# Optimization experiments

Measured on AMD Instinct MI355X. Metric: run time of the kernel, lower is better.

The kernel has to match this reference:

```python
import jax, jax.numpy as jnp
import numpy as np

M = 8192          # flattened tokens (batch*seq)
IN_FEATURES = 4096
OUT_FEATURES = 4096


def setup_inputs() -> dict:
    key = jax.random.key(0)
    k1, k2, k3 = jax.random.split(key, 3)
    # int8-valued activations and weights, stored as int32 (values in [-128, 127])
    x = jax.random.randint(k1, (M, IN_FEATURES), -128, 128, dtype=jnp.int32)
    int_weight = jax.random.randint(k2, (OUT_FEATURES, IN_FEATURES), -128, 127, dtype=jnp.int32)
    bias = (jax.random.normal(k3, (OUT_FEATURES,), dtype=jnp.float32) * 0.02).astype(jnp.float16)
    return {"x": x, "int_weight": int_weight, "bias": bias}


def reference(x, int_weight, bias):
    # x.to(torch.int8); quik int8Matmul: int8 GEMM with int32 accumulation, out = x @ W^T
    x_i8 = x.astype(jnp.int8)
    w_i8 = int_weight.astype(jnp.int8)
    acc = jax.lax.dot_general(
        x_i8, w_i8,
        dimension_numbers=(((1,), (1,)), ((), ())),  # [M, K] x [N, K] -> [M, N]
        preferred_element_type=jnp.int32,
    )
    # .to(torch.float16) then bias add (fused epilogue target)
    return acc.astype(jnp.float16) + bias
```

## Files before the change

### kernel.cpp

```cpp
#include <hip/hip_runtime.h>

#define MDIM 8192
#define NDIM 4096
#define KDIM 4096
#define BM 256
#define BN 128
#define BK 128

typedef int v4i __attribute__((ext_vector_type(4)));
typedef int v16i __attribute__((ext_vector_type(16)));

__device__ __forceinline__ unsigned pack4(int x, int y, int z, int w) {
    return (unsigned)(x & 0xff) | ((unsigned)(y & 0xff) << 8) |
           ((unsigned)(z & 0xff) << 16) | ((unsigned)w << 24);
}

__global__ __launch_bounds__(256) void pack_tiled(const int* __restrict__ x,
                                                  const int* __restrict__ w,
                                                  uint4* __restrict__ xp,
                                                  uint4* __restrict__ wp) {
    __shared__ unsigned lds32[256 * 33];
    const int wg  = blockIdx.x;
    const int tid = threadIdx.x;
    const int kq   = tid & 31;
    const int rsub = tid >> 5;

    if (wg < 1024) {
        const int mtile = wg >> 5, kiter = wg & 31;
        const int* base = x + (size_t)(mtile * 256) * KDIM + kiter * 128;
#pragma unroll
        for (int it = 0; it < 32; ++it) {
            const int row = it * 8 + rsub;
            int4 v = *(const int4*)(base + (size_t)row * KDIM + kq * 4);
            lds32[row * 33 + kq] = pack4(v.x, v.y, v.z, v.w);
        }
        __syncthreads();
        uint4* dst = xp + (size_t)(mtile * 32 + kiter) * 2048;
#pragma unroll
        for (int it = 0; it < 8; ++it) {
            const int g = it * 256 + tid;
            const int kb = g >> 8, row = g & 255;
            const unsigned* p = &lds32[row * 33 + kb * 4];
            uint4 o;
            o.x = p[0]; o.y = p[1]; o.z = p[2]; o.w = p[3];
            dst[g] = o;
        }
    } else {
        const int ntile = (wg - 1024) >> 5, kiter = wg & 31;
        const int* base = w + (size_t)(ntile * 128) * KDIM + kiter * 128;
#pragma unroll
        for (int it = 0; it < 16; ++it) {
            const int row = it * 8 + rsub;
            int4 v = *(const int4*)(base + (size_t)row * KDIM + kq * 4);
            lds32[row * 33 + kq] = pack4(v.x, v.y, v.z, v.w);
        }
        __syncthreads();
        uint4* dst = wp + (size_t)(ntile * 32 + kiter) * 1024;
#pragma unroll
        for (int it = 0; it < 4; ++it) {
            const int g  = it * 256 + tid;
            const int ln = g & 63, h = g >> 6;
            const int wc2 = h >> 3, nt = (h >> 2) & 1, ks = h & 3;
            const int row = wc2 * 64 + nt * 32 + (ln & 31);
            const int kb  = 2 * ks + (ln >> 5);
            const unsigned* p = &lds32[row * 33 + kb * 4];
            uint4 o;
            o.x = p[0]; o.y = p[1]; o.z = p[2]; o.w = p[3];
            dst[g] = o;
        }
    }
}

template <bool PACKED>
__global__ __launch_bounds__(256, 2) void gemm_i8(const char* __restrict__ Ap,
                                                  const char* __restrict__ Bp,
                                                  const int* __restrict__ A32,
                                                  const int* __restrict__ B32,
                                                  const _Float16* __restrict__ bias,
                                                  _Float16* __restrict__ out) {
    __shared__ char lds[65536];

    const int tid  = threadIdx.x;
    const int lane = tid & 63;
    const int wave = tid >> 6;
    const int bm0 = blockIdx.y * BM;
    const int bn0 = blockIdx.x * BN;
    const int wr  = wave >> 1;
    const int wc  = wave & 1;
    const int l31 = lane & 31;
    const int kg  = lane >> 5;

    const char* apan = Ap + (size_t)blockIdx.y * (BM * KDIM) + lane * 16;
    const char* bpan = Bp + (size_t)blockIdx.x * (BN * KDIM) + wc * 8192 + lane * 16;

    int abase[4];
#pragma unroll
    for (int mt = 0; mt < 4; ++mt)
        abase[mt] = kg * 4096 + (wr * 128 + mt * 32 + l31) * 16;

    v16i acc[4][2];
#pragma unroll
    for (int mt = 0; mt < 4; ++mt)
#pragma unroll
        for (int nt = 0; nt < 2; ++nt)
#pragma unroll
            for (int i = 0; i < 16; ++i) acc[mt][nt][i] = 0;

    auto issueA = [&](char* buf, const char* pan) {
#pragma unroll
        for (int r = 0; r < 8; ++r) {
            const int c = r * 4 + wave;
            __builtin_amdgcn_global_load_lds(
                (__attribute__((address_space(1))) void*)(pan + c * 1024),
                (__attribute__((address_space(3))) void*)(buf + c * 1024), 16, 0, 0);
        }
    };
    auto loadB = [&](v4i (&bf)[2][4], const char* pan) {
#pragma unroll
        for (int nt = 0; nt < 2; ++nt)
#pragma unroll
            for (int ks = 0; ks < 4; ++ks)
                bf[nt][ks] = *(const v4i*)(pan + (nt * 4 + ks) * 1024);
    };
    auto compute = [&](const char* buf, const v4i (&bf)[2][4]) {
#pragma unroll
        for (int ks = 0; ks < 4; ++ks) {
            v4i af[4];
#pragma unroll
            for (int mt = 0; mt < 4; ++mt)
                af[mt] = *(const v4i*)(buf + abase[mt] + ks * 8192);
#pragma unroll
            for (int mt = 0; mt < 4; ++mt)
#pragma unroll
                for (int nt = 0; nt < 2; ++nt)
                    acc[mt][nt] = __builtin_amdgcn_mfma_i32_32x32x32_i8(
                        af[mt], bf[nt][ks], acc[mt][nt], 0, 0, 0);
        }
    };

    if constexpr (PACKED) {
        v4i bf0[2][4], bf1[2][4];
        issueA(lds, apan);
        apan += BM * BK;
        loadB(bf0, bpan);
        bpan += BN * BK;
#pragma unroll 1
        for (int p = 0; p < 15; ++p) {
            __syncthreads();
            issueA(lds + 32768, apan);
            apan += BM * BK;
            loadB(bf1, bpan);
            bpan += BN * BK;
            compute(lds, bf0);
            __syncthreads();
            issueA(lds, apan);
            apan += BM * BK;
            loadB(bf0, bpan);
            bpan += BN * BK;
            compute(lds + 32768, bf1);
        }
        __syncthreads();
        issueA(lds + 32768, apan);
        loadB(bf1, bpan);
        compute(lds, bf0);
        __syncthreads();
        compute(lds + 32768, bf1);
    } else {
        int aoffs[8];
#pragma unroll
        for (int r = 0; r < 8; ++r) {
            const int c = r * 4 + wave;
            aoffs[r] = (bm0 + (c & 3) * 64 + lane) * KDIM + (c >> 2) * 16;
        }
        for (int k0 = 0; k0 < KDIM; k0 += BK) {
            v4i bfx[2][4];
#pragma unroll
            for (int r = 0; r < 8; ++r) {
                const int c = r * 4 + wave;
                const int4* s = (const int4*)(A32 + (size_t)aoffs[r]);
                int4 v0 = s[0], v1 = s[1], v2 = s[2], v3 = s[3];
                uint4 pk;
                pk.x = pack4(v0.x, v0.y, v0.z, v0.w);
                pk.y = pack4(v1.x, v1.y, v1.z, v1.w);
                pk.z = pack4(v2.x, v2.y, v2.z, v2.w);
                pk.w = pack4(v3.x, v3.y, v3.z, v3.w);
                *(uint4*)(lds + c * 1024 + lane * 16) = pk;
                aoffs[r] += BK;
            }
#pragma unroll
            for (int nt = 0; nt < 2; ++nt)
#pragma unroll
                for (int ks = 0; ks < 4; ++ks) {
                    const int* s = B32 + (size_t)(bn0 + wc * 64 + nt * 32 + l31) * KDIM
                                   + k0 + (2 * ks + kg) * 16;
                    int4 v0 = ((const int4*)s)[0], v1 = ((const int4*)s)[1];
                    int4 v2 = ((const int4*)s)[2], v3 = ((const int4*)s)[3];
                    bfx[nt][ks][0] = (int)pack4(v0.x, v0.y, v0.z, v0.w);
                    bfx[nt][ks][1] = (int)pack4(v1.x, v1.y, v1.z, v1.w);
                    bfx[nt][ks][2] = (int)pack4(v2.x, v2.y, v2.z, v2.w);
                    bfx[nt][ks][3] = (int)pack4(v3.x, v3.y, v3.z, v3.w);
                }
            __syncthreads();
            compute(lds, bfx);
            __syncthreads();
        }
    }

    const _Float16 bv0 = bias[bn0 + wc * 64 + l31];
    const _Float16 bv1 = bias[bn0 + wc * 64 + 32 + l31];
#pragma unroll
    for (int mt = 0; mt < 4; ++mt) {
#pragma unroll
        for (int nt = 0; nt < 2; ++nt) {
            const int gcol = bn0 + wc * 64 + nt * 32 + l31;
            const _Float16 bb = nt ? bv1 : bv0;
#pragma unroll
            for (int r = 0; r < 16; ++r) {
                const int rit  = (r & 3) + 8 * (r >> 2) + 4 * kg;
                const int grow = bm0 + wr * 128 + mt * 32 + rit;
                _Float16 h = (_Float16)(float)acc[mt][nt][r] + bb;
                out[(size_t)grow * NDIM + gcol] = h;
            }
        }
    }
}

extern "C" void kernel_launch(void* const* d_in, const int* in_sizes, int n_in,
                              void* d_out, int out_size, void* d_ws, size_t ws_size,
                              hipStream_t stream) {
    const int* x = (const int*)d_in[0];
    const int* w = (const int*)d_in[1];
    const _Float16* bias = (const _Float16*)d_in[2];
    _Float16* out = (_Float16*)d_out;

    const size_t xbytes = (size_t)MDIM * KDIM;
    const size_t wbytes = (size_t)NDIM * KDIM;

    if (ws_size >= xbytes + wbytes) {
        char* xp = (char*)d_ws;
        char* wp = xp + xbytes;
        pack_tiled<<<2048, 256, 0, stream>>>(x, w, (uint4*)xp, (uint4*)wp);
        gemm_i8<true><<<dim3(NDIM / BN, MDIM / BM), 256, 0, stream>>>(
            xp, wp, nullptr, nullptr, bias, out);
    } else {
        gemm_i8<false><<<dim3(NDIM / BN, MDIM / BM), 256, 0, stream>>>(
            nullptr, nullptr, x, w, bias, out);
    }
}
```

Baseline: 399.0 us.

## Split K-tile prefetch into quarters with vmcnt-gated barriers and MFMA priority

The packed GEMM main loop now interleaves prefetching of the next A tile (global-to-LDS loads) and B fragments in four quarter-slices, each followed by its matching quarter of MFMA work. The full __syncthreads is replaced by inline s_waitcnt vmcnt(N) plus s_barrier, so each quarter waits only for its own loads. s_setprio raises wave priority around the MFMA bursts. The aim is to hide memory latency more finely and cut barrier stalls. In exchange, correctness now depends on exact vmcnt counting and on the reuse timing of the double buffer.

```diff
diff --git a/kernel.cpp b/kernel.cpp
--- a/kernel.cpp
+++ b/kernel.cpp
@@ -78,7 +78,7 @@
                                                   const int* __restrict__ B32,
                                                   const _Float16* __restrict__ bias,
                                                   _Float16* __restrict__ out) {
-    __shared__ char lds[65536];
+    __shared__ __align__(16) char lds[65536];
 
     const int tid  = threadIdx.x;
     const int lane = tid & 63;
@@ -106,66 +106,82 @@
 #pragma unroll
             for (int i = 0; i < 16; ++i) acc[mt][nt][i] = 0;
 
-    auto issueA = [&](char* buf, const char* pan) {
-#pragma unroll
-        for (int r = 0; r < 8; ++r) {
-            const int c = r * 4 + wave;
-            __builtin_amdgcn_global_load_lds(
-                (__attribute__((address_space(1))) void*)(pan + c * 1024),
-                (__attribute__((address_space(3))) void*)(buf + c * 1024), 16, 0, 0);
-        }
-    };
-    auto loadB = [&](v4i (&bf)[2][4], const char* pan) {
-#pragma unroll
-        for (int nt = 0; nt < 2; ++nt)
-#pragma unroll
-            for (int ks = 0; ks < 4; ++ks)
-                bf[nt][ks] = *(const v4i*)(pan + (nt * 4 + ks) * 1024);
-    };
-    auto compute = [&](const char* buf, const v4i (&bf)[2][4]) {
-#pragma unroll
-        for (int ks = 0; ks < 4; ++ks) {
+    if constexpr (PACKED) {
+        v4i bf0[2][4], bf1[2][4];
+
+        auto prefq = [&](char* nbuf, v4i (&bfn)[2][4], int q) {
+#pragma unroll
+            for (int r2 = 0; r2 < 2; ++r2) {
+                const int c = (2 * q + r2) * 4 + wave;
+                __builtin_amdgcn_global_load_lds(
+                    (__attribute__((address_space(1))) void*)(apan + c * 1024),
+                    (__attribute__((address_space(3))) void*)(nbuf + c * 1024), 16, 0, 0);
+            }
+            bfn[0][q] = *(const v4i*)(bpan + q * 1024);
+            bfn[1][q] = *(const v4i*)(bpan + (4 + q) * 1024);
+        };
+        auto compq = [&](const char* cbuf, const v4i (&bfc)[2][4], int q) {
             v4i af[4];
 #pragma unroll
             for (int mt = 0; mt < 4; ++mt)
-                af[mt] = *(const v4i*)(buf + abase[mt] + ks * 8192);
+                af[mt] = *(const v4i*)(cbuf + abase[mt] + q * 8192);
+            __builtin_amdgcn_s_setprio(1);
 #pragma unroll
             for (int mt = 0; mt < 4; ++mt)
 #pragma unroll
                 for (int nt = 0; nt < 2; ++nt)
                     acc[mt][nt] = __builtin_amdgcn_mfma_i32_32x32x32_i8(
-                        af[mt], bf[nt][ks], acc[mt][nt], 0, 0, 0);
-        }
-    };
-
-    if constexpr (PACKED) {
-        v4i bf0[2][4], bf1[2][4];
-        issueA(lds, apan);
+                        af[mt], bfc[nt][q], acc[mt][nt], 0, 0, 0);
+            __builtin_amdgcn_s_setprio(0);
+        };
+
+#define WB(N) asm volatile("s_waitcnt vmcnt(" #N ")\n\ts_barrier" ::: "memory")
+
+#pragma unroll
+        for (int q = 0; q < 4; ++q) prefq(lds, bf0, q);
         apan += BM * BK;
-        loadB(bf0, bpan);
         bpan += BN * BK;
+
 #pragma unroll 1
         for (int p = 0; p < 15; ++p) {
-            __syncthreads();
-            issueA(lds + 32768, apan);
+            prefq(lds + 32768, bf1, 0); WB(16); compq(lds, bf0, 0);
+            prefq(lds + 32768, bf1, 1); WB(16); compq(lds, bf0, 1);
+            prefq(lds + 32768, bf1, 2); WB(16); compq(lds, bf0, 2);
+            prefq(lds + 32768, bf1, 3); WB(16); compq(lds, bf0, 3);
             apan += BM * BK;
-            loadB(bf1, bpan);
             bpan += BN * BK;
-            compute(lds, bf0);
-            __syncthreads();
-            issueA(lds, apan);
+            prefq(lds, bf0, 0); WB(16); compq(lds + 32768, bf1, 0);
+            prefq(lds, bf0, 1); WB(16); compq(lds + 32768, bf1, 1);
+            prefq(lds, bf0, 2); WB(16); compq(lds + 32768, bf1, 2);
+            prefq(lds, bf0, 3); WB(16); compq(lds + 32768, bf1, 3);
             apan += BM * BK;
-            loadB(bf0, bpan);
             bpan += BN * BK;
-            compute(lds + 32768, bf1);
-        }
-        __syncthreads();
-        issueA(lds + 32768, apan);
-        loadB(bf1, bpan);
-        compute(lds, bf0);
-        __syncthreads();
-        compute(lds + 32768, bf1);
+        }
+        prefq(lds + 32768, bf1, 0); WB(16); compq(lds, bf0, 0);
+        prefq(lds + 32768, bf1, 1); WB(16); compq(lds, bf0, 1);
+        prefq(lds + 32768, bf1, 2); WB(16); compq(lds, bf0, 2);
+        prefq(lds + 32768, bf1, 3); WB(16); compq(lds, bf0, 3);
+        WB(12); compq(lds + 32768, bf1, 0);
+        WB(8);  compq(lds + 32768, bf1, 1);
+        WB(4);  compq(lds + 32768, bf1, 2);
+        WB(0);  compq(lds + 32768, bf1, 3);
+#undef WB
     } else {
+        auto compute = [&](const char* buf, const v4i (&bf)[2][4]) {
+#pragma unroll
+            for (int ks = 0; ks < 4; ++ks) {
+                v4i af[4];
+#pragma unroll
+                for (int mt = 0; mt < 4; ++mt)
+                    af[mt] = *(const v4i*)(buf + abase[mt] + ks * 8192);
+#pragma unroll
+                for (int mt = 0; mt < 4; ++mt)
+#pragma unroll
+                    for (int nt = 0; nt < 2; ++nt)
+                        acc[mt][nt] = __builtin_amdgcn_mfma_i32_32x32x32_i8(
+                            af[mt], bf[nt][ks], acc[mt][nt], 0, 0, 0);
+            }
+        };
         int aoffs[8];
 #pragma unroll
         for (int r = 0; r < 8; ++r) {
```

New measurement: 386.5 us. -3.1%, faster.

## Rewrite int8 GEMM as 256x256 tile, 8-wave, 8-phase LDS-pipelined kernel

Applied to the files above, without the earlier changes.

Grows the GEMM tile to 256x256 and uses 512 threads (8 waves). A and B are both staged into a double-buffered 128KB LDS through global_load_lds, and each K tile is split into four barrier-separated MFMA clusters with s_setprio and explicit waitcnt. Blocks are remapped with a swizzled grid order for L2 locality, and the pack kernel now packs W in the same row-tiled layout as X. The aim is to cut global traffic per FLOP and overlap loads with MFMA work. The cost is more barriers, higher LDS and register pressure, and lower occupancy.

```diff
diff --git a/kernel.cpp b/kernel.cpp
--- a/kernel.cpp
+++ b/kernel.cpp
@@ -4,7 +4,7 @@
 #define NDIM 4096
 #define KDIM 4096
 #define BM 256
-#define BN 128
+#define BN 256
 #define BK 128
 
 typedef int v4i __attribute__((ext_vector_type(4)));
@@ -25,74 +25,191 @@
     const int kq   = tid & 31;
     const int rsub = tid >> 5;
 
+    const int* src;
+    uint4* dst;
     if (wg < 1024) {
         const int mtile = wg >> 5, kiter = wg & 31;
-        const int* base = x + (size_t)(mtile * 256) * KDIM + kiter * 128;
-#pragma unroll
-        for (int it = 0; it < 32; ++it) {
-            const int row = it * 8 + rsub;
-            int4 v = *(const int4*)(base + (size_t)row * KDIM + kq * 4);
-            lds32[row * 33 + kq] = pack4(v.x, v.y, v.z, v.w);
-        }
-        __syncthreads();
-        uint4* dst = xp + (size_t)(mtile * 32 + kiter) * 2048;
-#pragma unroll
-        for (int it = 0; it < 8; ++it) {
-            const int g = it * 256 + tid;
-            const int kb = g >> 8, row = g & 255;
-            const unsigned* p = &lds32[row * 33 + kb * 4];
-            uint4 o;
-            o.x = p[0]; o.y = p[1]; o.z = p[2]; o.w = p[3];
-            dst[g] = o;
-        }
+        src = x + (size_t)(mtile * 256) * KDIM + kiter * 128;
+        dst = xp + (size_t)(mtile * 32 + kiter) * 2048;
     } else {
         const int ntile = (wg - 1024) >> 5, kiter = wg & 31;
-        const int* base = w + (size_t)(ntile * 128) * KDIM + kiter * 128;
-#pragma unroll
-        for (int it = 0; it < 16; ++it) {
-            const int row = it * 8 + rsub;
-            int4 v = *(const int4*)(base + (size_t)row * KDIM + kq * 4);
-            lds32[row * 33 + kq] = pack4(v.x, v.y, v.z, v.w);
-        }
-        __syncthreads();
-        uint4* dst = wp + (size_t)(ntile * 32 + kiter) * 1024;
-#pragma unroll
-        for (int it = 0; it < 4; ++it) {
-            const int g  = it * 256 + tid;
-            const int ln = g & 63, h = g >> 6;
-            const int wc2 = h >> 3, nt = (h >> 2) & 1, ks = h & 3;
-            const int row = wc2 * 64 + nt * 32 + (ln & 31);
-            const int kb  = 2 * ks + (ln >> 5);
-            const unsigned* p = &lds32[row * 33 + kb * 4];
-            uint4 o;
-            o.x = p[0]; o.y = p[1]; o.z = p[2]; o.w = p[3];
-            dst[g] = o;
-        }
-    }
-}
-
-template <bool PACKED>
-__global__ __launch_bounds__(256, 2) void gemm_i8(const char* __restrict__ Ap,
-                                                  const char* __restrict__ Bp,
-                                                  const int* __restrict__ A32,
-                                                  const int* __restrict__ B32,
-                                                  const _Float16* __restrict__ bias,
-                                                  _Float16* __restrict__ out) {
-    __shared__ char lds[65536];
+        src = w + (size_t)(ntile * 256) * KDIM + kiter * 128;
+        dst = wp + (size_t)(ntile * 32 + kiter) * 2048;
+    }
+#pragma unroll
+    for (int it = 0; it < 32; ++it) {
+        const int row = it * 8 + rsub;
+        int4 v = *(const int4*)(src + (size_t)row * KDIM + kq * 4);
+        lds32[row * 33 + kq] = pack4(v.x, v.y, v.z, v.w);
+    }
+    __syncthreads();
+#pragma unroll
+    for (int it = 0; it < 8; ++it) {
+        const int g = it * 256 + tid;
+        const int kb = g >> 8, row = g & 255;
+        const unsigned* p = &lds32[row * 33 + kb * 4];
+        uint4 o;
+        o.x = p[0]; o.y = p[1]; o.z = p[2]; o.w = p[3];
+        dst[g] = o;
+    }
+}
+
+__global__ __launch_bounds__(512, 2) void gemm_i8_8ph(const char* __restrict__ Ap,
+                                                      const char* __restrict__ Bp,
+                                                      const _Float16* __restrict__ bias,
+                                                      _Float16* __restrict__ out) {
+    __shared__ __align__(16) char lds[131072];
 
     const int tid  = threadIdx.x;
     const int lane = tid & 63;
     const int wave = tid >> 6;
-    const int bm0 = blockIdx.y * BM;
-    const int bn0 = blockIdx.x * BN;
+    const int wr   = wave >> 2;
+    const int wcn  = wave & 3;
+    const int l31  = lane & 31;
+    const int kg   = lane >> 5;
+
+    const int lid = blockIdx.y * 16 + blockIdx.x;
+    const int xc  = lid & 7, ii = lid >> 3;
+    const int bx  = (xc & 3) * 4 + (ii & 3);
+    const int by  = (xc >> 2) * 16 + (ii >> 2);
+    const int bm0 = by * BM;
+    const int bn0 = bx * BN;
+
+    const char* apan = Ap + (size_t)by * (BM * KDIM) + tid * 16;
+    const char* bpan = Bp + (size_t)bx * (BN * KDIM) + tid * 16;
+
+    int aoff[4], boff[2];
+#pragma unroll
+    for (int mt = 0; mt < 4; ++mt)
+        aoff[mt] = kg * 4096 + (wr * 128 + mt * 32 + l31) * 16;
+#pragma unroll
+    for (int nt = 0; nt < 2; ++nt)
+        boff[nt] = kg * 4096 + (wcn * 64 + nt * 32 + l31) * 16;
+
+    v16i acc[4][2];
+#pragma unroll
+    for (int mt = 0; mt < 4; ++mt)
+#pragma unroll
+        for (int nt = 0; nt < 2; ++nt)
+#pragma unroll
+            for (int i = 0; i < 16; ++i) acc[mt][nt][i] = 0;
+
+    auto stageA = [&](int nb, const char* p) {
+#pragma unroll
+        for (int c2 = 0; c2 < 4; ++c2)
+            __builtin_amdgcn_global_load_lds(
+                (__attribute__((address_space(1))) const void*)(p + c2 * 8192),
+                (__attribute__((address_space(3))) void*)(lds + nb + c2 * 8192 + tid * 16),
+                16, 0, 0);
+    };
+    auto stageB = [&](int nb, const char* p) {
+#pragma unroll
+        for (int c2 = 0; c2 < 4; ++c2)
+            __builtin_amdgcn_global_load_lds(
+                (__attribute__((address_space(1))) const void*)(p + c2 * 8192),
+                (__attribute__((address_space(3))) void*)(lds + nb + 32768 + c2 * 8192 + tid * 16),
+                16, 0, 0);
+    };
+
+    v4i af[8], bf[4];
+    auto ldsub = [&](int base, int mp, int nth) {
+        if (nth == 0) {
+#pragma unroll
+            for (int m2 = 0; m2 < 2; ++m2)
+#pragma unroll
+                for (int ks = 0; ks < 4; ++ks)
+                    af[m2 * 4 + ks] =
+                        *(const v4i*)(lds + base + ks * 8192 + aoff[mp * 2 + m2]);
+        }
+#pragma unroll
+        for (int ks = 0; ks < 4; ++ks)
+            bf[ks] = *(const v4i*)(lds + base + 32768 + ks * 8192 + boff[nth]);
+    };
+    auto cluster = [&](int mp, int nth) {
+        __builtin_amdgcn_s_setprio(1);
+#pragma unroll
+        for (int ks = 0; ks < 4; ++ks)
+#pragma unroll
+            for (int m2 = 0; m2 < 2; ++m2)
+                acc[mp * 2 + m2][nth] = __builtin_amdgcn_mfma_i32_32x32x32_i8(
+                    af[m2 * 4 + ks], bf[ks], acc[mp * 2 + m2][nth], 0, 0, 0);
+        __builtin_amdgcn_s_setprio(0);
+    };
+
+#define BAR   __builtin_amdgcn_s_barrier()
+#define LGKM0 do { asm volatile("s_waitcnt lgkmcnt(0)" ::: "memory"); \
+                   __builtin_amdgcn_sched_barrier(0); } while (0)
+#define VM0   asm volatile("s_waitcnt vmcnt(0)" ::: "memory")
+
+    auto tile = [&](int base, int nb, bool stg) {
+        ldsub(base, 0, 0);
+        if (stg) stageA(nb, apan);
+        BAR; LGKM0; cluster(0, 0); BAR;
+        ldsub(base, 0, 1);
+        if (stg) stageB(nb, bpan);
+        BAR; LGKM0; cluster(0, 1); BAR;
+        ldsub(base, 1, 0);
+        BAR; LGKM0; cluster(1, 0); BAR;
+        ldsub(base, 1, 1);
+        BAR; LGKM0; cluster(1, 1);
+        if (stg) VM0;
+        BAR;
+    };
+
+    stageA(0, apan);
+    stageB(0, bpan);
+    apan += BM * BK;
+    bpan += BN * BK;
+    VM0; BAR;
+
+#pragma unroll 1
+    for (int t2 = 0; t2 < 15; ++t2) {
+        tile(0, 65536, true);
+        apan += BM * BK; bpan += BN * BK;
+        tile(65536, 0, true);
+        apan += BM * BK; bpan += BN * BK;
+    }
+    tile(0, 65536, true);
+    tile(65536, 0, false);
+
+#undef BAR
+#undef LGKM0
+#undef VM0
+
+    const _Float16 bv0 = bias[bn0 + wcn * 64 + l31];
+    const _Float16 bv1 = bias[bn0 + wcn * 64 + 32 + l31];
+#pragma unroll
+    for (int mt = 0; mt < 4; ++mt) {
+#pragma unroll
+        for (int nt = 0; nt < 2; ++nt) {
+            const int gcol = bn0 + wcn * 64 + nt * 32 + l31;
+            const _Float16 bb = nt ? bv1 : bv0;
+#pragma unroll
+            for (int r = 0; r < 16; ++r) {
+                const int rit  = (r & 3) + 8 * (r >> 2) + 4 * kg;
+                const int grow = bm0 + wr * 128 + mt * 32 + rit;
+                _Float16 h = (_Float16)(float)acc[mt][nt][r] + bb;
+                out[(size_t)grow * NDIM + gcol] = h;
+            }
+        }
+    }
+}
+
+__global__ __launch_bounds__(256, 2) void gemm_i8_fb(const int* __restrict__ A32,
+                                                     const int* __restrict__ B32,
+                                                     const _Float16* __restrict__ bias,
+                                                     _Float16* __restrict__ out) {
+    __shared__ char lds[32768];
+    const int tid  = threadIdx.x;
+    const int lane = tid & 63;
+    const int wave = tid >> 6;
+    const int bm0 = blockIdx.y * 256;
+    const int bn0 = blockIdx.x * 128;
     const int wr  = wave >> 1;
     const int wc  = wave & 1;
     const int l31 = lane & 31;
     const int kg  = lane >> 5;
 
-    const char* apan = Ap + (size_t)blockIdx.y * (BM * KDIM) + lane * 16;
-    const char* bpan = Bp + (size_t)blockIdx.x * (BN * KDIM) + wc * 8192 + lane * 16;
-
     int abase[4];
 #pragma unroll
     for (int mt = 0; mt < 4; ++mt)
@@ -106,104 +223,55 @@
 #pragma unroll
             for (int i = 0; i < 16; ++i) acc[mt][nt][i] = 0;
 
-    auto issueA = [&](char* buf, const char* pan) {
+    int aoffs[8];
+#pragma unroll
+    for (int r = 0; r < 8; ++r) {
+        const int c = r * 4 + wave;
+        aoffs[r] = (bm0 + (c & 3) * 64 + lane) * KDIM + (c >> 2) * 16;
+    }
+    for (int k0 = 0; k0 < KDIM; k0 += 128) {
+        v4i bfx[2][4];
 #pragma unroll
         for (int r = 0; r < 8; ++r) {
             const int c = r * 4 + wave;
-            __builtin_amdgcn_global_load_lds(
-                (__attribute__((address_space(1))) void*)(pan + c * 1024),
-                (__attribute__((address_space(3))) void*)(buf + c * 1024), 16, 0, 0);
-        }
-    };
-    auto loadB = [&](v4i (&bf)[2][4], const char* pan) {
+            const int4* s = (const int4*)(A32 + (size_t)aoffs[r]);
+            int4 v0 = s[0], v1 = s[1], v2 = s[2], v3 = s[3];
+            uint4 pk;
+            pk.x = pack4(v0.x, v0.y, v0.z, v0.w);
+            pk.y = pack4(v1.x, v1.y, v1.z, v1.w);
+            pk.z = pack4(v2.x, v2.y, v2.z, v2.w);
+            pk.w = pack4(v3.x, v3.y, v3.z, v3.w);
+            *(uint4*)(lds + c * 1024 + lane * 16) = pk;
+            aoffs[r] += 128;
+        }
 #pragma unroll
         for (int nt = 0; nt < 2; ++nt)
 #pragma unroll
-            for (int ks = 0; ks < 4; ++ks)
-                bf[nt][ks] = *(const v4i*)(pan + (nt * 4 + ks) * 1024);
-    };
-    auto compute = [&](const char* buf, const v4i (&bf)[2][4]) {
+            for (int ks = 0; ks < 4; ++ks) {
+                const int* s = B32 + (size_t)(bn0 + wc * 64 + nt * 32 + l31) * KDIM
+                               + k0 + (2 * ks + kg) * 16;
+                int4 v0 = ((const int4*)s)[0], v1 = ((const int4*)s)[1];
+                int4 v2 = ((const int4*)s)[2], v3 = ((const int4*)s)[3];
+                bfx[nt][ks][0] = (int)pack4(v0.x, v0.y, v0.z, v0.w);
+                bfx[nt][ks][1] = (int)pack4(v1.x, v1.y, v1.z, v1.w);
+                bfx[nt][ks][2] = (int)pack4(v2.x, v2.y, v2.z, v2.w);
+                bfx[nt][ks][3] = (int)pack4(v3.x, v3.y, v3.z, v3.w);
+            }
+        __syncthreads();
 #pragma unroll
         for (int ks = 0; ks < 4; ++ks) {
-            v4i af[4];
+            v4i afr[4];
 #pragma unroll
             for (int mt = 0; mt < 4; ++mt)
-                af[mt] = *(const v4i*)(buf + abase[mt] + ks * 8192);
+                afr[mt] = *(const v4i*)(lds + abase[mt] + ks * 8192);
 #pragma unroll
             for (int mt = 0; mt < 4; ++mt)
 #pragma unroll
                 for (int nt = 0; nt < 2; ++nt)
                     acc[mt][nt] = __builtin_amdgcn_mfma_i32_32x32x32_i8(
-                        af[mt], bf[nt][ks], acc[mt][nt], 0, 0, 0);
-        }
-    };
-
-    if constexpr (PACKED) {
-        v4i bf0[2][4], bf1[2][4];
-        issueA(lds, apan);
-        apan += BM * BK;
-        loadB(bf0, bpan);
-        bpan += BN * BK;
-#pragma unroll 1
-        for (int p = 0; p < 15; ++p) {
-            __syncthreads();
-            issueA(lds + 32768, apan);
-            apan += BM * BK;
-            loadB(bf1, bpan);
-            bpan += BN * BK;
-            compute(lds, bf0);
-            __syncthreads();
-            issueA(lds, apan);
-            apan += BM * BK;
-            loadB(bf0, bpan);
-            bpan += BN * BK;
-            compute(lds + 32768, bf1);
+                        afr[mt], bfx[nt][ks], acc[mt][nt], 0, 0, 0);
         }
         __syncthreads();
-        issueA(lds + 32768, apan);
-        loadB(bf1, bpan);
-        compute(lds, bf0);
-        __syncthreads();
-        compute(lds + 32768, bf1);
-    } else {
-        int aoffs[8];
-#pragma unroll
-        for (int r = 0; r < 8; ++r) {
-            const int c = r * 4 + wave;
-            aoffs[r] = (bm0 + (c & 3) * 64 + lane) * KDIM + (c >> 2) * 16;
-        }
-        for (int k0 = 0; k0 < KDIM; k0 += BK) {
-            v4i bfx[2][4];
-#pragma unroll
-            for (int r = 0; r < 8; ++r) {
-                const int c = r * 4 + wave;
-                const int4* s = (const int4*)(A32 + (size_t)aoffs[r]);
-                int4 v0 = s[0], v1 = s[1], v2 = s[2], v3 = s[3];
-                uint4 pk;
-                pk.x = pack4(v0.x, v0.y, v0.z, v0.w);
-                pk.y = pack4(v1.x, v1.y, v1.z, v1.w);
-                pk.z = pack4(v2.x, v2.y, v2.z, v2.w);
-                pk.w = pack4(v3.x, v3.y, v3.z, v3.w);
-                *(uint4*)(lds + c * 1024 + lane * 16) = pk;
-                aoffs[r] += BK;
-            }
-#pragma unroll
-            for (int nt = 0; nt < 2; ++nt)
-#pragma unroll
-                for (int ks = 0; ks < 4; ++ks) {
-                    const int* s = B32 + (size_t)(bn0 + wc * 64 + nt * 32 + l31) * KDIM
-                                   + k0 + (2 * ks + kg) * 16;
-                    int4 v0 = ((const int4*)s)[0], v1 = ((const int4*)s)[1];
-                    int4 v2 = ((const int4*)s)[2], v3 = ((const int4*)s)[3];
-                    bfx[nt][ks][0] = (int)pack4(v0.x, v0.y, v0.z, v0.w);
-                    bfx[nt][ks][1] = (int)pack4(v1.x, v1.y, v1.z, v1.w);
-                    bfx[nt][ks][2] = (int)pack4(v2.x, v2.y, v2.z, v2.w);
-                    bfx[nt][ks][3] = (int)pack4(v3.x, v3.y, v3.z, v3.w);
-                }
-            __syncthreads();
-            compute(lds, bfx);
-            __syncthreads();
-        }
     }
 
     const _Float16 bv0 = bias[bn0 + wc * 64 + l31];
@@ -239,11 +307,11 @@
     if (ws_size >= xbytes + wbytes) {
         char* xp = (char*)d_ws;
         char* wp = xp + xbytes;
-        pack_tiled<<<2048, 256, 0, stream>>>(x, w, (uint4*)xp, (uint4*)wp);
-        gemm_i8<true><<<dim3(NDIM / BN, MDIM / BM), 256, 0, stream>>>(
-            xp, wp, nullptr, nullptr, bias, out);
+        pack_tiled<<<1536, 256, 0, stream>>>(x, w, (uint4*)xp, (uint4*)wp);
+        gemm_i8_8ph<<<dim3(NDIM / BN, MDIM / BM), 512, 0, stream>>>(
+            (const char*)xp, (const char*)wp, bias, out);
     } else {
-        gemm_i8<false><<<dim3(NDIM / BN, MDIM / BM), 256, 0, stream>>>(
-            nullptr, nullptr, x, w, bias, out);
-    }
-}
+        gemm_i8_fb<<<dim3(NDIM / 128, MDIM / 256), 256, 0, stream>>>(
+            x, w, bias, out);
+    }
+}
```

Measured after the change: 388.5 us. -2.6%, faster.
